# Kernel tuning notes

Measured on AMD Instinct MI355X. Metric: run time of the kernel, lower is better.

## Reference

```python
import jax, jax.numpy as jnp
import numpy as np

M_BUCKETS = 2048  # input_features // q = 4096 // 2


def countsketch(x, hash_idx, rand_sgn, m=M_BUCKETS):
    # x: [N, D]; scatter-add signed columns into m buckets -> [N, m]
    return jnp.zeros((x.shape[0], m), x.dtype).at[:, hash_idx].add(x * rand_sgn[None, :])


def setup_inputs() -> dict:
    key = jax.random.key(0)
    k1, k2, k3, k4, k5 = jax.random.split(key, 5)
    B, D, O = 4096, 4096, 4096
    inp = jax.random.normal(k1, (B, D), dtype=jnp.float32)
    # match torch init: weight uniform(-sqrt(3)/sqrt(D), sqrt(3)/sqrt(D)), bias uniform(-1/sqrt(D), 1/sqrt(D))
    bound = 1.0 / np.sqrt(D)
    weight = jax.random.uniform(k2, (O, D), dtype=jnp.float32,
                                minval=-bound * np.sqrt(3.0), maxval=bound * np.sqrt(3.0))
    bias = jax.random.uniform(k3, (O,), dtype=jnp.float32, minval=-bound, maxval=bound)
    hash_idx = jax.random.randint(k4, (D,), 0, M_BUCKETS, dtype=jnp.int32)
    rand_sgn = (2.0 * jax.random.randint(k5, (D,), 0, 2).astype(jnp.float32) - 1.0)
    return {"input": inp, "weight": weight, "bias": bias,
            "hash_idx": hash_idx, "rand_sgn": rand_sgn}


def reference(input, weight, bias, hash_idx, rand_sgn):
    input_sketch = countsketch(input, hash_idx, rand_sgn)    # [B, m]
    weight_sketch = countsketch(weight, hash_idx, rand_sgn)  # [O, m]
    out = input_sketch @ weight_sketch.T + bias[None, :]     # [B, O]
    return out
```

## Files before the change

kernel.cpp:

```cpp
#include <hip/hip_runtime.h>
#include <hip/hip_bf16.h>
#include <stdint.h>

#define D_DIM     4096
#define MB        2048
#define NROWS     4096
#define K_DIM     MB

typedef __bf16 bf16x8 __attribute__((ext_vector_type(8)));
typedef float  floatx4 __attribute__((ext_vector_type(4)));

__device__ __forceinline__ void gld_lds16(const void* g, void* l) {
    __builtin_amdgcn_global_load_lds(
        (const __attribute__((address_space(1))) unsigned int*)g,
        (__attribute__((address_space(3))) unsigned int*)l,
        16, 0, 0);
}

__global__ __launch_bounds__(256) void build_csr(
    const int* __restrict__ hash_idx,
    unsigned int* __restrict__ desc,
    unsigned short* __restrict__ perm16)
{
    __shared__ int cnt[MB];
    __shared__ int scan[MB];
    const int t = threadIdx.x;

    for (int k = t; k < MB; k += 256) cnt[k] = 0;
    __syncthreads();
    for (int j = t; j < D_DIM; j += 256) atomicAdd(&cnt[hash_idx[j]], 1);
    __syncthreads();
    for (int k = t; k < MB; k += 256) scan[k] = cnt[k];
    __syncthreads();
    for (int stride = 1; stride < MB; stride <<= 1) {
        int vals[8];
        #pragma unroll
        for (int i = 0; i < 8; ++i) {
            int k = t + 256 * i;
            vals[i] = (k >= stride) ? scan[k - stride] : 0;
        }
        __syncthreads();
        #pragma unroll
        for (int i = 0; i < 8; ++i) scan[t + 256 * i] += vals[i];
        __syncthreads();
    }
    for (int k = t; k < MB; k += 256) {
        int excl = scan[k] - cnt[k];
        desc[k] = ((unsigned)excl << 16) | (unsigned)cnt[k];
        cnt[k] = excl;
    }
    __syncthreads();
    for (int j = t; j < D_DIM; j += 256) {
        int k = hash_idx[j];
        int pos = atomicAdd(&cnt[k], 1);
        perm16[pos] = (unsigned short)j;
    }
}

__global__ __launch_bounds__(256) void sketch_gather(
    const float* __restrict__ input,
    const float* __restrict__ weight,
    const float* __restrict__ rand_sgn,
    const unsigned int* __restrict__ desc,
    const unsigned short* __restrict__ perm16,
    __hip_bfloat16* __restrict__ sk_in,
    __hip_bfloat16* __restrict__ sk_w)
{
    __shared__ __align__(16) float rv0[D_DIM + 8];
    __shared__ __align__(16) float rv1[D_DIM + 8];
    __shared__ __align__(16) unsigned short perm[D_DIM];
    const int b = blockIdx.x;
    const bool is_w = (b >= NROWS / 2);
    const int pr = is_w ? (b - NROWS / 2) : b;
    const float* src = (is_w ? weight : input) + (size_t)pr * 2 * D_DIM;
    __hip_bfloat16* dst = (is_w ? sk_w : sk_in) + (size_t)pr * 2 * MB;
    const int t = threadIdx.x;

    const uint4* pg = (const uint4*)perm16;
    ((uint4*)perm)[t]       = pg[t];
    ((uint4*)perm)[t + 256] = pg[t + 256];

    const float4* s4 = (const float4*)src;
    const float4* g4 = (const float4*)rand_sgn;
    #pragma unroll
    for (int i = 0; i < 4; ++i) {
        int q = t + 256 * i;
        float4 g = g4[q];
        float4 x0 = s4[q], x1 = s4[q + 1024];
        float4 y0; y0.x = x0.x*g.x; y0.y = x0.y*g.y; y0.z = x0.z*g.z; y0.w = x0.w*g.w;
        float4 y1; y1.x = x1.x*g.x; y1.y = x1.y*g.y; y1.z = x1.z*g.z; y1.w = x1.w*g.w;
        *(float4*)&rv0[4 * q] = y0;
        *(float4*)&rv1[4 * q] = y1;
    }
    __syncthreads();

    float4 a0[4], a1[4];
    #pragma unroll
    for (int i = 0; i < 4; ++i) {
        int q = t + 256 * i;
        ushort4 pp = *(const ushort4*)&perm[4 * q];
        a0[i].x = rv0[pp.x]; a0[i].y = rv0[pp.y];
        a0[i].z = rv0[pp.z]; a0[i].w = rv0[pp.w];
        a1[i].x = rv1[pp.x]; a1[i].y = rv1[pp.y];
        a1[i].z = rv1[pp.z]; a1[i].w = rv1[pp.w];
    }
    __syncthreads();
    #pragma unroll
    for (int i = 0; i < 4; ++i) {
        int q = t + 256 * i;
        *(float4*)&rv0[4 * q] = a0[i];
        *(float4*)&rv1[4 * q] = a1[i];
    }
    __syncthreads();

    #pragma unroll
    for (int i = 0; i < 8; ++i) {
        int k = t + 256 * i;
        unsigned d = desc[k];
        int st = (int)(d >> 16), c = (int)(d & 0xFFFF);
        float s0 = 0.f, s1 = 0.f;
        #pragma unroll
        for (int j = 0; j < 8; ++j) {
            float v0 = rv0[st + j], v1 = rv1[st + j];
            bool m = (j < c);
            s0 += m ? v0 : 0.f;
            s1 += m ? v1 : 0.f;
        }
        for (int j = 8; j < c; ++j) {
            s0 += rv0[st + j]; s1 += rv1[st + j];
        }
        dst[k]      = __float2bfloat16(s0);
        dst[MB + k] = __float2bfloat16(s1);
    }
}

#define LDSA(p, h) (lds + (p)*32768 + (h)*16384)
#define LDSB(p, h) (lds + 65536 + (p)*32768 + (h)*16384)
#define SWZ(L) ((L) ^ ((((L) >> 7) & 7) << 4))

#define BAR() __builtin_amdgcn_s_barrier()
#define VMCNT4() asm volatile("s_waitcnt vmcnt(4)" ::: "memory")

#define STAGE_A(p, mh, kt) do { \
    int L_ = (mh)*8192 + t*16; \
    int P_ = SWZ(L_); \
    const char* s_ = Ab + (size_t)(rowBase + (P_ >> 7)) * 4096 \
                        + (size_t)((((kt) & 31) * 128) + (P_ & 127)); \
    gld_lds16(s_,                       LDSA(p, 0) + L_); \
    gld_lds16(s_ + (size_t)128 * 4096,  LDSA(p, 1) + L_); \
} while (0)

#define STAGE_B(p, nh, kt) do { \
    int L_ = (t >> 8) * 8192 + (nh)*4096 + (t & 255) * 16; \
    int P_ = SWZ(L_); \
    const char* s_ = Bb + (size_t)(colBase + (P_ >> 7)) * 4096 \
                        + (size_t)((((kt) & 31) * 128) + (P_ & 127)); \
    gld_lds16(s_,                       LDSB(p, 0) + L_); \
    gld_lds16(s_ + (size_t)128 * 4096,  LDSB(p, 1) + L_); \
} while (0)

#define LOAD_A(p, mh) do { \
    const char* ba_ = LDSA(p, wm); \
    _Pragma("unroll") \
    for (int i_ = 0; i_ < 4; ++i_) { \
        int r_ = (mh)*64 + i_*16 + mrow; \
        _Pragma("unroll") \
        for (int kk_ = 0; kk_ < 2; ++kk_) { \
            int L_ = r_*128 + kk_*64 + quad*16; \
            af[i_][kk_] = *(const bf16x8*)(ba_ + SWZ(L_)); \
        } \
    } \
} while (0)

#define LOAD_B(p, nh, BF) do { \
    const char* bb_ = LDSB(p, wn >> 1); \
    _Pragma("unroll") \
    for (int j_ = 0; j_ < 2; ++j_) { \
        int r_ = (wn & 1)*64 + (nh)*32 + j_*16 + mrow; \
        _Pragma("unroll") \
        for (int kk_ = 0; kk_ < 2; ++kk_) { \
            int L_ = r_*128 + kk_*64 + quad*16; \
            BF[j_][kk_] = *(const bf16x8*)(bb_ + SWZ(L_)); \
        } \
    } \
} while (0)

#define MFMA_Q(mh, nh, BF) do { \
    __builtin_amdgcn_s_setprio(1); \
    _Pragma("unroll") \
    for (int kk_ = 0; kk_ < 2; ++kk_) \
        _Pragma("unroll") \
        for (int i_ = 0; i_ < 4; ++i_) \
            _Pragma("unroll") \
            for (int j_ = 0; j_ < 2; ++j_) \
                acc[(mh)*4 + i_][(nh)*2 + j_] = \
                    __builtin_amdgcn_mfma_f32_16x16x32_bf16( \
                        af[i_][kk_], BF[j_][kk_], \
                        acc[(mh)*4 + i_][(nh)*2 + j_], 0, 0, 0); \
    __builtin_amdgcn_s_setprio(0); \
} while (0)

__global__ __launch_bounds__(512, 2) void gemm_bt_bias(
    const __hip_bfloat16* __restrict__ A,
    const __hip_bfloat16* __restrict__ B,
    const float* __restrict__ bias,
    float* __restrict__ C)
{
    __shared__ __align__(16) char lds[131072];
    const char* Ab = (const char*)A;
    const char* Bb = (const char*)B;

    const int t = threadIdx.x;
    const int lane = t & 63;
    const int wid  = t >> 6;
    const int wm = wid >> 2;
    const int wn = wid & 3;
    const int quad = lane >> 4;
    const int mrow = lane & 15;

    const int lid  = blockIdx.y * 16 + blockIdx.x;
    const int xcd  = lid & 7;
    const int slot = lid >> 3;
    const int bx   = (xcd & 1) * 8 + (slot & 7);
    const int by   = (xcd >> 1) * 4 + (slot >> 3);
    const int rowBase = by * 256;
    const int colBase = bx * 256;

    bf16x8 af[4][2];
    bf16x8 bfr0[2][2];
    bf16x8 bfr1[2][2];
    floatx4 acc[8][4];
    const floatx4 zero = {0.f, 0.f, 0.f, 0.f};
    #pragma unroll
    for (int i = 0; i < 8; ++i)
        #pragma unroll
        for (int j = 0; j < 4; ++j) acc[i][j] = zero;

    STAGE_A(0, 0, 0); STAGE_B(0, 1, 0); STAGE_B(0, 0, 0); STAGE_A(0, 1, 0);
    STAGE_A(1, 0, 1); STAGE_B(1, 1, 1);
    VMCNT4();
    BAR();

    #pragma unroll 1
    for (int it = 0; it < 16; ++it) {
        const int kt = 2 * it;
        LOAD_A(0, 0); LOAD_B(0, 0, bfr0); STAGE_B(1, 0, kt + 1);
        MFMA_Q(0, 0, bfr0); BAR();
        LOAD_B(0, 1, bfr1); STAGE_A(1, 1, kt + 1);
        MFMA_Q(0, 1, bfr1); BAR();
        LOAD_A(0, 1); STAGE_A(0, 0, kt + 2);
        MFMA_Q(1, 1, bfr1); BAR();
        STAGE_B(0, 1, kt + 2);
        MFMA_Q(1, 0, bfr0); VMCNT4(); BAR();
        LOAD_A(1, 0); LOAD_B(1, 0, bfr0); STAGE_B(0, 0, kt + 2);
        MFMA_Q(0, 0, bfr0); BAR();
        LOAD_B(1, 1, bfr1); STAGE_A(0, 1, kt + 2);
        MFMA_Q(0, 1, bfr1); BAR();
        LOAD_A(1, 1); STAGE_A(1, 0, kt + 3);
        MFMA_Q(1, 1, bfr1); BAR();
        STAGE_B(1, 1, kt + 3);
        MFMA_Q(1, 0, bfr0); VMCNT4(); BAR();
    }

    float bj[4];
    #pragma unroll
    for (int j = 0; j < 4; ++j)
        bj[j] = bias[colBase + wn * 64 + j * 16 + mrow];
    #pragma unroll
    for (int i = 0; i < 8; ++i) {
        int m0 = rowBase + wm * 128 + i * 16 + quad * 4;
        #pragma unroll
        for (int j = 0; j < 4; ++j) {
            int n = colBase + wn * 64 + j * 16 + mrow;
            #pragma unroll
            for (int p = 0; p < 4; ++p)
                C[(size_t)(m0 + p) * NROWS + n] = acc[i][j][p] + bj[j];
        }
    }
}

extern "C" void kernel_launch(void* const* d_in, const int* in_sizes, int n_in,
                              void* d_out, int out_size, void* d_ws, size_t ws_size,
                              hipStream_t stream) {
    const float* input  = (const float*)d_in[0];
    const float* weight = (const float*)d_in[1];
    const float* bias   = (const float*)d_in[2];
    const int*   hidx   = (const int*)d_in[3];
    const float* sgn    = (const float*)d_in[4];
    float* out = (float*)d_out;

    char* ws = (char*)d_ws;
    __hip_bfloat16* sk_in = (__hip_bfloat16*)ws;
    __hip_bfloat16* sk_w  = (__hip_bfloat16*)(ws + (size_t)16 * 1024 * 1024);
    unsigned int*   desc  = (unsigned int*)(ws + (size_t)32 * 1024 * 1024);
    unsigned short* perm16 = (unsigned short*)(ws + (size_t)32 * 1024 * 1024 + 8192);

    build_csr<<<1, 256, 0, stream>>>(hidx, desc, perm16);
    sketch_gather<<<NROWS, 256, 0, stream>>>(input, weight, sgn, desc, perm16,
                                             sk_in, sk_w);
    gemm_bt_bias<<<dim3(16, 16), 512, 0, stream>>>(sk_in, sk_w, bias, out);
}
```

Baseline: 249.4 us.

## Regroup GEMM main loop stages to halve barriers per iteration

Reorders the software-pipelined MFMA main loop so that both global-to-LDS stages for a half-step are issued together, LDS fragment loads are batched, and two MFMA quadrants run back-to-back between barriers. This cuts the workgroup barriers per iteration from eight to four, aiming to reduce sync stalls and give the scheduler longer MFMA runs to hide LDS and global latency. The risk is that the changed issue order alters what the VMCNT waits cover, and that batching fragment loads raises register pressure or leaves the MFMA units idle while loads are outstanding.

```diff
diff --git a/kernel.cpp b/kernel.cpp
--- a/kernel.cpp
+++ b/kernel.cpp
@@ -244,22 +244,22 @@
     #pragma unroll 1
     for (int it = 0; it < 16; ++it) {
         const int kt = 2 * it;
-        LOAD_A(0, 0); LOAD_B(0, 0, bfr0); STAGE_B(1, 0, kt + 1);
-        MFMA_Q(0, 0, bfr0); BAR();
-        LOAD_B(0, 1, bfr1); STAGE_A(1, 1, kt + 1);
-        MFMA_Q(0, 1, bfr1); BAR();
-        LOAD_A(0, 1); STAGE_A(0, 0, kt + 2);
-        MFMA_Q(1, 1, bfr1); BAR();
-        STAGE_B(0, 1, kt + 2);
-        MFMA_Q(1, 0, bfr0); VMCNT4(); BAR();
-        LOAD_A(1, 0); LOAD_B(1, 0, bfr0); STAGE_B(0, 0, kt + 2);
-        MFMA_Q(0, 0, bfr0); BAR();
-        LOAD_B(1, 1, bfr1); STAGE_A(0, 1, kt + 2);
-        MFMA_Q(0, 1, bfr1); BAR();
-        LOAD_A(1, 1); STAGE_A(1, 0, kt + 3);
-        MFMA_Q(1, 1, bfr1); BAR();
-        STAGE_B(1, 1, kt + 3);
-        MFMA_Q(1, 0, bfr0); VMCNT4(); BAR();
+        STAGE_B(1, 0, kt + 1); STAGE_A(1, 1, kt + 1);
+        LOAD_A(0, 0); LOAD_B(0, 0, bfr0); LOAD_B(0, 1, bfr1);
+        MFMA_Q(0, 0, bfr0); MFMA_Q(0, 1, bfr1);
+        BAR();
+        STAGE_A(0, 0, kt + 2); STAGE_B(0, 1, kt + 2);
+        LOAD_A(0, 1);
+        MFMA_Q(1, 1, bfr1); MFMA_Q(1, 0, bfr0);
+        VMCNT4(); BAR();
+        STAGE_B(0, 0, kt + 2); STAGE_A(0, 1, kt + 2);
+        LOAD_A(1, 0); LOAD_B(1, 0, bfr0); LOAD_B(1, 1, bfr1);
+        MFMA_Q(0, 0, bfr0); MFMA_Q(0, 1, bfr1);
+        BAR();
+        STAGE_A(1, 0, kt + 3); STAGE_B(1, 1, kt + 3);
+        LOAD_A(1, 1);
+        MFMA_Q(1, 1, bfr1); MFMA_Q(1, 0, bfr0);
+        VMCNT4(); BAR();
     }
 
     float bj[4];
```

Measured after the change: 251.9 us. Within noise of the previous version (+1.0%).
